# Kernel optimization log

Measured on AMD Instinct MI355X. Metric: run time of the kernel, lower is better.

Reference implementation:

```python
import jax, jax.numpy as jnp
import numpy as np

N_PROT, N_SUB = 50000, 2000
D_PROT, D_SUB, D_PROJ, KERNEL, N_INT = 256, 256, 128, 16, 64


def setup_inputs() -> dict:
    key = jax.random.key(0)
    ks = jax.random.split(key, 8)
    init = lambda k, shape: jax.random.normal(k, shape, dtype=jnp.float32) * 0.02
    return {
        "prot_node": jax.random.normal(ks[0], (N_PROT, D_PROT), dtype=jnp.float32),
        "sub_node": jax.random.normal(ks[1], (N_SUB, D_SUB), dtype=jnp.float32),
        "int_index": jax.random.randint(ks[2], (N_INT,), 0, N_SUB),
        "Wp": init(ks[3], (D_PROT, D_PROJ)),  # prot_proj weight (in,out layout)
        "bp": jnp.zeros((D_PROJ,), jnp.float32),
        "Ws": init(ks[4], (D_SUB, D_PROJ)),   # sub_proj weight
        "bs": jnp.zeros((D_PROJ,), jnp.float32),
        "wa": init(ks[5], (2 * D_PROJ,)),     # attention_proj weight (out dim 1)
        "ba": jnp.zeros((), jnp.float32),
        "sub_out": init(ks[6], (D_PROJ, D_SUB)),
        "prot_out": init(ks[7], (D_PROJ, D_PROT)),
    }


def reference(prot_node, sub_node, int_index, Wp, bp, Ws, bs, wa, ba, sub_out, prot_out):
    K = KERNEL
    prot_proj = prot_node @ Wp + bp                              # [N, D]
    # reaction potion: sum of projected interacting substrate nodes -> [D]
    reaction = jnp.sum(sub_node[int_index] @ Ws + bs, axis=0)
    num_windows = prot_node.shape[0] - K + 1                     # W
    # attention_proj(concat(window_row, reaction)) splits linearly:
    #   logit = window_row . wa[:D] + reaction . wa[D:] + ba
    # The reaction part is a per-row constant -> compute per-node logits once.
    w1, w2 = wa[:D_PROJ], wa[D_PROJ:]
    g = prot_proj @ w1 + (reaction @ w2 + ba)                    # [N]
    # sliding-window gather indices [W, K]
    idx = jnp.arange(num_windows)[:, None] + jnp.arange(K)[None, :]
    attn = jax.nn.softmax(g[idx], axis=1)                        # [W, K] softmax over window
    local = jnp.einsum('wk,wkd->wd', attn, prot_proj[idx])       # [W, D]
    scores = local + reaction                                    # [W, D]
    # rank windows and pick the best
    top = jnp.argmax(jnp.sum(scores, axis=1))
    top_score = scores[top]                                      # [D]
    # scatter updates back into the node features
    # (set matches torch's non-accumulating fancy-index += for duplicate indices;
    #  the added delta is identical for every row anyway)
    sub_new = sub_node.at[int_index].set(sub_node[int_index] + top_score @ sub_out)
    prot_delta = top_score @ prot_out                            # [D_PROT]
    win = jax.lax.dynamic_slice(prot_node, (top, 0), (K, D_PROT))
    prot_new = jax.lax.dynamic_update_slice(prot_node, win + prot_delta, (top, 0))
    return prot_new, sub_new, int_index
```

## Files before the change

kernel.cpp:

```cpp
#include <hip/hip_runtime.h>
#include <math.h>

#define N_PROT 50000
#define N_SUB  2000
#define D_PROT 256
#define D_SUB  256
#define D_PROJ 128
#define KW     16
#define N_INT  64
#define NWIN   (N_PROT - KW + 1)

#define OUT_SUB (N_PROT * D_PROT)
#define OUT_IDX (OUT_SUB + N_SUB * D_SUB)

#define WS_PACK  0
#define WS_REACT 2
#define WS_CNT   130
#define WS_U1    132
#define WS_U2    388
#define WS_G     644
#define WS_P     (WS_G + N_PROT)

#define PB 1563
#define SB 64
#define NBLK (PB + SB)
#define WBLK ((NWIN + 1023) / 1024)

__global__ __launch_bounds__(256) void k_prep(
    const float* __restrict__ sub_node, const int* __restrict__ int_index,
    const float* __restrict__ Ws, const float* __restrict__ bs,
    const float* __restrict__ Wp, const float* __restrict__ wa,
    float* __restrict__ ws) {
  const int tid = threadIdx.x;
  if (blockIdx.x == 0) {
    __shared__ int   sidx[N_INT];
    __shared__ float ssum[D_SUB];
    if (tid < N_INT) sidx[tid] = int_index[tid];
    __syncthreads();
    float acc = 0.f;
    #pragma unroll 8
    for (int i = 0; i < N_INT; ++i) acc += sub_node[sidx[i] * D_SUB + tid];
    ssum[tid] = acc;
    __syncthreads();
    if (tid < D_PROJ) {
      float r = 64.0f * bs[tid];
      #pragma unroll 8
      for (int d = 0; d < D_SUB; ++d) r = fmaf(ssum[d], Ws[d * D_PROJ + tid], r);
      ws[WS_REACT + tid] = r;
    }
    if (tid == 0) {
      *((unsigned long long*)ws) = 0ull;
      ((unsigned int*)ws)[WS_CNT] = 0u;
    }
  } else {
    __shared__ float swa[D_PROJ];
    if (tid < D_PROJ) swa[tid] = wa[tid];
    __syncthreads();
    float s1 = 0.f, s2 = 0.f;
    const float4* wrow = (const float4*)&Wp[tid * D_PROJ];
    #pragma unroll 8
    for (int j4 = 0; j4 < D_PROJ / 4; ++j4) {
      float4 w = wrow[j4];
      float4 a = *(const float4*)&swa[j4 * 4];
      s1 = fmaf(w.x, a.x, fmaf(w.y, a.y, fmaf(w.z, a.z, fmaf(w.w, a.w, s1))));
      s2 += w.x + w.y + w.z + w.w;
    }
    ws[WS_U1 + tid] = s1;
    ws[WS_U2 + tid] = s2;
  }
}

__global__ __launch_bounds__(256) void k_main(
    const float* __restrict__ prot, const float* __restrict__ sub_node,
    const int* __restrict__ int_index, float* __restrict__ out,
    float* __restrict__ ws) {
  const int tid = threadIdx.x, lane = tid & 63, wave = tid >> 6;
  const int b = blockIdx.x;
  if (b < PB) {
    const float4 c1 = *(const float4*)&ws[WS_U1 + lane * 4];
    const float4 c2 = *(const float4*)&ws[WS_U2 + lane * 4];
    const int rbase = b * 32 + wave * 8;
    if (rbase + 8 <= N_PROT) {
      float4 av[8];
      #pragma unroll
      for (int i = 0; i < 8; ++i)
        av[i] = *(const float4*)&prot[(rbase + i) * D_PROT + lane * 4];
      #pragma unroll
      for (int i = 0; i < 8; ++i)
        *(float4*)&out[(rbase + i) * D_PROT + lane * 4] = av[i];
      #pragma unroll
      for (int i = 0; i < 8; ++i) {
        float g = av[i].x * c1.x + av[i].y * c1.y + av[i].z * c1.z + av[i].w * c1.w;
        float p = av[i].x * c2.x + av[i].y * c2.y + av[i].z * c2.z + av[i].w * c2.w;
        #pragma unroll
        for (int off = 32; off > 0; off >>= 1) {
          g += __shfl_xor(g, off, 64);
          p += __shfl_xor(p, off, 64);
        }
        if (lane == 0) {
          const int r = rbase + i;
          ws[WS_G + r] = g; ws[WS_P + r] = p;
        }
      }
    } else {
      for (int i = 0; i < 8; ++i) {
        const int r = rbase + i;
        if (r >= N_PROT) break;
        const float4 av = *(const float4*)&prot[r * D_PROT + lane * 4];
        *(float4*)&out[r * D_PROT + lane * 4] = av;
        float g = av.x * c1.x + av.y * c1.y + av.z * c1.z + av.w * c1.w;
        float p = av.x * c2.x + av.y * c2.y + av.z * c2.z + av.w * c2.w;
        for (int off = 32; off > 0; off >>= 1) {
          g += __shfl_xor(g, off, 64);
          p += __shfl_xor(p, off, 64);
        }
        if (lane == 0) { ws[WS_G + r] = g; ws[WS_P + r] = p; }
      }
    }
  } else {
    const int sb = b - PB;
    #pragma unroll
    for (int i = 0; i < 8; ++i) {
      const int gi = sb * 2048 + i * 256 + tid;
      if (gi < (N_SUB * D_SUB) / 4)
        *(float4*)&out[OUT_SUB + gi * 4] = *(const float4*)&sub_node[gi * 4];
    }
    if (sb == 0 && tid < N_INT) out[OUT_IDX + tid] = (float)int_index[tid];
  }
}

__global__ __launch_bounds__(1024) void k_finish(
    const float* __restrict__ prot, const float* __restrict__ sub_node,
    const int* __restrict__ int_index, const float* __restrict__ Wp,
    const float* __restrict__ bp, const float* __restrict__ sub_out,
    const float* __restrict__ prot_out, float* __restrict__ ws,
    float* __restrict__ out) {
  __shared__ float sg[1024 + KW], sp[1024 + KW];
  __shared__ unsigned long long wred[16];
  __shared__ int slast;
  const int tid = threadIdx.x;
  const int w0 = blockIdx.x * 1024;
  for (int i = tid; i < 1024 + KW - 1; i += 1024) {
    int idx = w0 + i;
    bool ok = idx < N_PROT;
    sg[i] = ok ? ws[WS_G + idx] : -1e30f;
    sp[i] = ok ? ws[WS_P + idx] : 0.f;
  }
  __syncthreads();
  {
    int w = w0 + tid;
    unsigned long long best = 0ull;
    if (w < NWIN) {
      float m = sg[tid];
      #pragma unroll
      for (int k = 1; k < KW; ++k) m = fmaxf(m, sg[tid + k]);
      float s = 0.f, t = 0.f;
      #pragma unroll
      for (int k = 0; k < KW; ++k) {
        float e = expf(sg[tid + k] - m);
        s += e;
        t = fmaf(e, sp[tid + k], t);
      }
      t /= s;
      unsigned int bb = __float_as_uint(t);
      unsigned int u = bb ^ ((bb & 0x80000000u) ? 0xFFFFFFFFu : 0x80000000u);
      best = ((unsigned long long)u << 32) |
             (unsigned long long)(0xFFFFFFFFu - (unsigned)w);
    }
    #pragma unroll
    for (int off = 32; off > 0; off >>= 1) {
      unsigned long long o = __shfl_xor(best, off, 64);
      if (o > best) best = o;
    }
    if ((tid & 63) == 0) wred[tid >> 6] = best;
  }
  __syncthreads();
  if (tid == 0) {
    unsigned long long b2 = wred[0];
    for (int i = 1; i < 16; ++i) if (wred[i] > b2) b2 = wred[i];
    atomicMax((unsigned long long*)ws, b2);
    __threadfence();
    unsigned int ticket = atomicAdd(&((unsigned int*)ws)[WS_CNT], 1u);
    slast = (ticket == WBLK - 1) ? 1 : 0;
  }
  __syncthreads();
  if (!slast) return;

  __shared__ float aprot[KW][D_PROT];
  __shared__ float attn[KW];
  __shared__ float v[D_PROT];
  __shared__ float part[8][D_PROJ];
  __shared__ float ts[D_PROJ];
  __shared__ float partP[4][D_PROT], partS[4][D_PROT];
  __shared__ float pdelta[D_PROT], sdelta[D_SUB];
  __shared__ int   sidx[N_INT];
  __shared__ int   swtop;
  if (tid == 0) {
    unsigned long long pk = atomicMax((unsigned long long*)ws, 0ull);
    swtop = (int)(0xFFFFFFFFu - (unsigned)(pk & 0xFFFFFFFFull));
  }
  __syncthreads();
  const int wtop = swtop;
  {
    const int row = tid >> 6, c4 = (tid & 63) * 4;
    *(float4*)&aprot[row][c4] = *(const float4*)&prot[(wtop + row) * D_PROT + c4];
  }
  if (tid < N_INT) sidx[tid] = int_index[tid];
  if (tid == 0) {
    float m = ws[WS_G + wtop];
    for (int k = 1; k < KW; ++k) m = fmaxf(m, ws[WS_G + wtop + k]);
    float e[KW], s = 0.f;
    for (int k = 0; k < KW; ++k) { e[k] = expf(ws[WS_G + wtop + k] - m); s += e[k]; }
    for (int k = 0; k < KW; ++k) attn[k] = e[k] / s;
  }
  __syncthreads();
  if (tid < D_PROT) {
    float a = 0.f;
    #pragma unroll
    for (int k = 0; k < KW; ++k) a = fmaf(attn[k], aprot[k][tid], a);
    v[tid] = a;
  }
  __syncthreads();
  {
    const int j = tid & 127, s = tid >> 7;
    float p = 0.f;
    const float* wp = Wp + (s * 32) * D_PROJ + j;
    #pragma unroll 8
    for (int d = 0; d < 32; ++d) p = fmaf(v[s * 32 + d], wp[d * D_PROJ], p);
    part[s][j] = p;
  }
  __syncthreads();
  if (tid < D_PROJ) {
    float a = ws[WS_REACT + tid] + bp[tid];
    #pragma unroll
    for (int s = 0; s < 8; ++s) a += part[s][tid];
    ts[tid] = a;
  }
  __syncthreads();
  {
    const int d = tid & 255, s = tid >> 8;
    float pp = 0.f, ss = 0.f;
    #pragma unroll 8
    for (int j = 0; j < 32; ++j) {
      const float t = ts[s * 32 + j];
      pp = fmaf(t, prot_out[(s * 32 + j) * D_PROT + d], pp);
      ss = fmaf(t, sub_out[(s * 32 + j) * D_SUB + d], ss);
    }
    partP[s][d] = pp; partS[s][d] = ss;
  }
  __syncthreads();
  if (tid < D_PROT) {
    pdelta[tid] = partP[0][tid] + partP[1][tid] + partP[2][tid] + partP[3][tid];
    sdelta[tid] = partS[0][tid] + partS[1][tid] + partS[2][tid] + partS[3][tid];
  }
  __syncthreads();
  {
    const int row = tid >> 6, c4 = (tid & 63) * 4;
    float4 a = *(float4*)&aprot[row][c4];
    float4 d = *(float4*)&pdelta[c4];
    a.x += d.x; a.y += d.y; a.z += d.z; a.w += d.w;
    *(float4*)&out[(wtop + row) * D_PROT + c4] = a;
  }
  #pragma unroll
  for (int it = 0; it < 4; ++it) {
    const int f = tid + it * 1024;
    const int row = f >> 6, c4 = (f & 63) * 4;
    const int rr = sidx[row];
    float4 sv = *(const float4*)&sub_node[rr * D_SUB + c4];
    float4 d = *(float4*)&sdelta[c4];
    sv.x += d.x; sv.y += d.y; sv.z += d.z; sv.w += d.w;
    *(float4*)&out[OUT_SUB + rr * D_SUB + c4] = sv;
  }
}

extern "C" void kernel_launch(void* const* d_in, const int* in_sizes, int n_in,
                              void* d_out, int out_size, void* d_ws, size_t ws_size,
                              hipStream_t stream) {
  const float* prot     = (const float*)d_in[0];
  const float* sub      = (const float*)d_in[1];
  const int*   idx      = (const int*)d_in[2];
  const float* Wp       = (const float*)d_in[3];
  const float* bp       = (const float*)d_in[4];
  const float* Ws       = (const float*)d_in[5];
  const float* bs       = (const float*)d_in[6];
  const float* wa       = (const float*)d_in[7];
  const float* sub_out  = (const float*)d_in[9];
  const float* prot_out = (const float*)d_in[10];
  float* out = (float*)d_out;
  float* ws  = (float*)d_ws;

  k_prep<<<2, 256, 0, stream>>>(sub, idx, Ws, bs, Wp, wa, ws);
  k_main<<<NBLK, 256, 0, stream>>>(prot, sub, idx, out, ws);
  k_finish<<<WBLK, 1024, 0, stream>>>(prot, sub, idx, Wp, bp, sub_out, prot_out,
                                      ws, out);
}
```

Before: 151.3 us.

## Stage protein rows in swizzled LDS tile and reduce dot products via shared memory

Replaces the per-row wavefront shuffle reductions in the streaming copy kernel with a block-wide scheme. Each block loads 32 rows, writes them to an XOR-swizzled LDS tile, and each thread computes partial dot products over 32 columns. Partials are combined through a shared reduction array. This removes the 12 cross-lane shuffles per row, at the cost of 32KB of LDS per block and two barriers, which may lower occupancy for a kernel that is bound by memory bandwidth.

```diff
diff --git a/kernel.cpp b/kernel.cpp
--- a/kernel.cpp
+++ b/kernel.cpp
@@ -21,6 +21,7 @@
 #define WS_G     644
 #define WS_P     (WS_G + N_PROT)
 
+#define RB 32
 #define PB 1563
 #define SB 64
 #define NBLK (PB + SB)
@@ -74,47 +75,73 @@
     const float* __restrict__ prot, const float* __restrict__ sub_node,
     const int* __restrict__ int_index, float* __restrict__ out,
     float* __restrict__ ws) {
-  const int tid = threadIdx.x, lane = tid & 63, wave = tid >> 6;
+  const int tid = threadIdx.x;
   const int b = blockIdx.x;
   if (b < PB) {
-    const float4 c1 = *(const float4*)&ws[WS_U1 + lane * 4];
-    const float4 c2 = *(const float4*)&ws[WS_U2 + lane * 4];
-    const int rbase = b * 32 + wave * 8;
-    if (rbase + 8 <= N_PROT) {
+    __shared__ float tile[RB * 256];
+    __shared__ float red[8][RB][2];
+    const int R0 = b * RB;
+    const int group = tid >> 5;
+    const int rloc  = tid & 31;
+    float4 u1v[8], u2v[8];
+    #pragma unroll
+    for (int c = 0; c < 8; ++c) {
+      u1v[c] = *(const float4*)&ws[WS_U1 + group * 32 + c * 4];
+      u2v[c] = *(const float4*)&ws[WS_U2 + group * 32 + c * 4];
+    }
+    const float* pr = prot + (long)R0 * D_PROT;
+    float*       po = out  + (long)R0 * D_PROT;
+    if (R0 + RB <= N_PROT) {
       float4 av[8];
       #pragma unroll
       for (int i = 0; i < 8; ++i)
-        av[i] = *(const float4*)&prot[(rbase + i) * D_PROT + lane * 4];
+        av[i] = *(const float4*)&pr[(tid + i * 256) * 4];
       #pragma unroll
       for (int i = 0; i < 8; ++i)
-        *(float4*)&out[(rbase + i) * D_PROT + lane * 4] = av[i];
+        *(float4*)&po[(tid + i * 256) * 4] = av[i];
       #pragma unroll
       for (int i = 0; i < 8; ++i) {
-        float g = av[i].x * c1.x + av[i].y * c1.y + av[i].z * c1.z + av[i].w * c1.w;
-        float p = av[i].x * c2.x + av[i].y * c2.y + av[i].z * c2.z + av[i].w * c2.w;
+        const int idx = tid + i * 256;
+        const int row = idx >> 6, col = idx & 63;
+        *(float4*)&tile[row * 256 + (col ^ row) * 4] = av[i];
+      }
+    } else {
+      #pragma unroll
+      for (int i = 0; i < 8; ++i) {
+        const int idx = tid + i * 256;
+        const int row = idx >> 6, col = idx & 63;
+        float4 av = make_float4(0.f, 0.f, 0.f, 0.f);
+        if (R0 + row < N_PROT) {
+          av = *(const float4*)&pr[idx * 4];
+          *(float4*)&po[idx * 4] = av;
+        }
+        *(float4*)&tile[row * 256 + (col ^ row) * 4] = av;
+      }
+    }
+    __syncthreads();
+    {
+      float g = 0.f, p = 0.f;
+      #pragma unroll
+      for (int c = 0; c < 8; ++c) {
+        const int q = group * 8 + c;
+        const float4 a = *(const float4*)&tile[rloc * 256 + (q ^ rloc) * 4];
+        g = fmaf(a.x, u1v[c].x, fmaf(a.y, u1v[c].y,
+            fmaf(a.z, u1v[c].z, fmaf(a.w, u1v[c].w, g))));
+        p = fmaf(a.x, u2v[c].x, fmaf(a.y, u2v[c].y,
+            fmaf(a.z, u2v[c].z, fmaf(a.w, u2v[c].w, p))));
+      }
+      red[group][rloc][0] = g;
+      red[group][rloc][1] = p;
+    }
+    __syncthreads();
+    if (tid < RB) {
+      const int r = R0 + tid;
+      if (r < N_PROT) {
+        float gg = 0.f, pp = 0.f;
         #pragma unroll
-        for (int off = 32; off > 0; off >>= 1) {
-          g += __shfl_xor(g, off, 64);
-          p += __shfl_xor(p, off, 64);
-        }
-        if (lane == 0) {
-          const int r = rbase + i;
-          ws[WS_G + r] = g; ws[WS_P + r] = p;
-        }
-      }
-    } else {
-      for (int i = 0; i < 8; ++i) {
-        const int r = rbase + i;
-        if (r >= N_PROT) break;
-        const float4 av = *(const float4*)&prot[r * D_PROT + lane * 4];
-        *(float4*)&out[r * D_PROT + lane * 4] = av;
-        float g = av.x * c1.x + av.y * c1.y + av.z * c1.z + av.w * c1.w;
-        float p = av.x * c2.x + av.y * c2.y + av.z * c2.z + av.w * c2.w;
-        for (int off = 32; off > 0; off >>= 1) {
-          g += __shfl_xor(g, off, 64);
-          p += __shfl_xor(p, off, 64);
-        }
-        if (lane == 0) { ws[WS_G + r] = g; ws[WS_P + r] = p; }
+        for (int s = 0; s < 8; ++s) { gg += red[s][tid][0]; pp += red[s][tid][1]; }
+        ws[WS_G + r] = gg;
+        ws[WS_P + r] = pp;
       }
     }
   } else {
```

Result: slower. 157.6 us (+4.2%).
